# Kernel tuning notes

Hardware: AMD Instinct MI355X
Metric: run time of the kernel (lower is better)

## Reference

```python
import jax, jax.numpy as jnp
import numpy as np

ALPHA = 0.02  # LeakyReLU slope used throughout the module


def _leaky(x):
    return jnp.where(x >= 0, x, ALPHA * x)


def setup_inputs() -> dict:
    key = jax.random.key(0)
    ks = jax.random.split(key, 6)
    N, NEIGH, D_IN, D_HID, D_OUT = 131072, 25, 128, 32, 32
    self_vecs = jax.random.normal(ks[0], (N, D_IN), dtype=jnp.float32)
    neigh_vecs = jax.random.normal(ks[1], (N, NEIGH, D_IN), dtype=jnp.float32)
    # mlp params: truncated_normal(stddev=0.001) in original; normal*0.001 is fine for a reference
    W_mlp = jax.random.normal(ks[2], (D_IN, D_HID), dtype=jnp.float32) * 0.001
    b_mlp = jax.random.normal(ks[3], (D_HID,), dtype=jnp.float32) * 0.001
    # glorot uniform range sqrt(6/(fan_in+fan_out))
    r_va = float(np.sqrt(6.0 / (D_HID + D_OUT)))
    W_va = jax.random.uniform(ks[4], (D_IN, D_OUT), dtype=jnp.float32, minval=-r_va, maxval=r_va)
    W_neigh = jax.random.uniform(ks[5], (D_HID, D_OUT), dtype=jnp.float32, minval=-r_va, maxval=r_va)
    return {"self_vecs": self_vecs, "neigh_vecs": neigh_vecs,
            "W_mlp": W_mlp, "b_mlp": b_mlp, "W_va": W_va, "W_neigh": W_neigh}


def reference(self_vecs, neigh_vecs, W_mlp, b_mlp, W_va, W_neigh):
    # MLP over each neighbor feature: [N, NEIGH, D_IN] -> [N, NEIGH, D_HID]
    h = _leaky(jnp.einsum('bnd,dh->bnh', neigh_vecs, W_mlp) + b_mlp)
    # max-pool over neighbor axis -> [N, D_HID]
    neigh_h = jnp.max(h, axis=1)
    # two bias-free projections, add, final activation
    out = _leaky(self_vecs @ W_va + neigh_h @ W_neigh)  # [N, D_OUT]
    return out
```

## Files before the change

### kernel.cpp

```cpp
#include <hip/hip_runtime.h>
#include <stdint.h>

typedef short bf16x8 __attribute__((ext_vector_type(8)));
typedef float f32x4  __attribute__((ext_vector_type(4)));

static constexpr float ALPHA = 0.02f;

__device__ __forceinline__ float leaky(float x) { return fmaxf(x, ALPHA * x); }

__device__ __forceinline__ unsigned swz(unsigned b) {
    unsigned n = (b >> 9) & 15u;
    return b ^ (n << 5) ^ (((n >> 2) & 1u) << 4);
}

__device__ __forceinline__ short f2bf(float f) {
    unsigned u = __builtin_bit_cast(unsigned, f);
    unsigned r = (u + 0x7FFFu + ((u >> 16) & 1u)) >> 16;
    return (short)r;
}

__device__ __forceinline__ void gload16(const void* g, void* l) {
    __builtin_amdgcn_global_load_lds(
        (const __attribute__((address_space(1))) unsigned*)g,
        (__attribute__((address_space(3))) unsigned*)l, 16, 0, 0);
}

__device__ __forceinline__ bf16x8 frag_from_lds(const char* base, unsigned L) {
    const float4 a = *(const float4*)(base + swz(L));
    const float4 b = *(const float4*)(base + swz(L + 16u));
    bf16x8 r;
    r[0] = f2bf(a.x); r[1] = f2bf(a.y); r[2] = f2bf(a.z); r[3] = f2bf(a.w);
    r[4] = f2bf(b.x); r[5] = f2bf(b.y); r[6] = f2bf(b.z); r[7] = f2bf(b.w);
    return r;
}

__global__ __launch_bounds__(64, 1)
void sage_mfma(const float* __restrict__ self_vecs,
               const float* __restrict__ xg,
               const float* __restrict__ W_mlp,
               const float* __restrict__ b_mlp,
               const float* __restrict__ W_va,
               const float* __restrict__ W_neigh,
               float* __restrict__ out, int N)
{
    __shared__ __align__(16) char  buf0[13312];
    __shared__ __align__(16) char  buf1[13312];
    __shared__ __align__(16) float nhbuf[16 * 36];

    const int lane = threadIdx.x & 63;
    const int n15  = lane & 15;
    const int g    = lane >> 4;
    const unsigned wid  = blockIdx.x;
    const unsigned row0 = wid * 16u;

    const unsigned xlimit = (unsigned)N * 12800u - 16u;

    {
        unsigned base = row0 * 12800u;
#pragma unroll
        for (int i = 0; i < 13; ++i) {
            unsigned dl  = (unsigned)(i * 1024 + lane * 16);
            unsigned src = base + swz(dl);
            src = src > xlimit ? xlimit : src;
            gload16((const char*)xg + src, buf0 + i * 1024);
        }
    }

    bf16x8 B1[2][4], B2[2][5];
#pragma unroll
    for (int ht = 0; ht < 2; ++ht) {
#pragma unroll
        for (int kt = 0; kt < 4; ++kt) {
            bf16x8 r1, r2;
#pragma unroll
            for (int j = 0; j < 8; ++j) {
                int k = kt * 32 + g * 8 + j;
                r1[j] = f2bf(W_mlp[k * 32 + ht * 16 + n15]);
                r2[j] = f2bf(W_va [k * 32 + ht * 16 + n15]);
            }
            B1[ht][kt] = r1; B2[ht][kt] = r2;
        }
        bf16x8 r3;
#pragma unroll
        for (int j = 0; j < 8; ++j)
            r3[j] = f2bf(W_neigh[(g * 8 + j) * 32 + ht * 16 + n15]);
        B2[ht][4] = r3;
    }
    const float bl = b_mlp[n15], bh = b_mlp[16 + n15];

    const f32x4 zero4 = {0.f, 0.f, 0.f, 0.f};

#pragma unroll 2
    for (int r = 0; r < 16; ++r) {
        char* cur = (r & 1) ? buf1 : buf0;
        char* nxt = (r & 1) ? buf0 : buf1;

        if (r < 15) {
            unsigned base = (row0 + (unsigned)r + 1u) * 12800u;
#pragma unroll
            for (int i = 0; i < 13; ++i) {
                unsigned dl  = (unsigned)(i * 1024 + lane * 16);
                unsigned src = base + swz(dl);
                src = src > xlimit ? xlimit : src;
                gload16((const char*)xg + src, nxt + i * 1024);
            }
            asm volatile("s_waitcnt vmcnt(13)" ::: "memory");
        } else {
            unsigned base = row0 * 512u;
#pragma unroll
            for (int i = 0; i < 8; ++i) {
                unsigned dl = (unsigned)(i * 1024 + lane * 16);
                gload16((const char*)self_vecs + base + swz(dl), buf0 + i * 1024);
            }
            asm volatile("s_waitcnt vmcnt(8)" ::: "memory");
        }
        __builtin_amdgcn_sched_barrier(0);

        f32x4 acc[2][2];
        acc[0][0] = zero4; acc[0][1] = zero4; acc[1][0] = zero4; acc[1][1] = zero4;

        const unsigned nA = (unsigned)n15;
        const unsigned nB = (unsigned)((n15 < 9) ? (16 + n15) : 8);

#pragma unroll
        for (int kt = 0; kt < 4; ++kt) {
            bf16x8 a = frag_from_lds(cur, nA * 512u + (unsigned)(kt * 128 + g * 32));
            acc[0][0] = __builtin_amdgcn_mfma_f32_16x16x32_bf16(a, B1[0][kt], acc[0][0], 0, 0, 0);
            acc[0][1] = __builtin_amdgcn_mfma_f32_16x16x32_bf16(a, B1[1][kt], acc[0][1], 0, 0, 0);
        }
#pragma unroll
        for (int kt = 0; kt < 4; ++kt) {
            bf16x8 a = frag_from_lds(cur, nB * 512u + (unsigned)(kt * 128 + g * 32));
            acc[1][0] = __builtin_amdgcn_mfma_f32_16x16x32_bf16(a, B1[0][kt], acc[1][0], 0, 0, 0);
            acc[1][1] = __builtin_amdgcn_mfma_f32_16x16x32_bf16(a, B1[1][kt], acc[1][1], 0, 0, 0);
        }

#pragma unroll
        for (int ht = 0; ht < 2; ++ht) {
            float m = -3.0e38f;
#pragma unroll
            for (int q = 0; q < 4; ++q) m = fmaxf(m, acc[0][ht][q]);
#pragma unroll
            for (int q = 0; q < 4; ++q) {
                float v = (g * 4 + q < 9) ? acc[1][ht][q] : -3.0e38f;
                m = fmaxf(m, v);
            }
            m = fmaxf(m, __shfl_xor(m, 16));
            m = fmaxf(m, __shfl_xor(m, 32));
            float nhv = leaky(m + (ht ? bh : bl));
            if (lane < 16) nhbuf[r * 36 + ht * 16 + n15] = nhv;
        }
    }

    asm volatile("s_waitcnt vmcnt(0)" ::: "memory");
    __builtin_amdgcn_sched_barrier(0);

    f32x4 acc2[2];
    acc2[0] = zero4; acc2[1] = zero4;

#pragma unroll
    for (int kt = 0; kt < 4; ++kt) {
        bf16x8 a = frag_from_lds(buf0, (unsigned)n15 * 512u + (unsigned)(kt * 128 + g * 32));
        acc2[0] = __builtin_amdgcn_mfma_f32_16x16x32_bf16(a, B2[0][kt], acc2[0], 0, 0, 0);
        acc2[1] = __builtin_amdgcn_mfma_f32_16x16x32_bf16(a, B2[1][kt], acc2[1], 0, 0, 0);
    }
    {
        const float4 p = *(const float4*)&nhbuf[n15 * 36 + g * 8];
        const float4 q = *(const float4*)&nhbuf[n15 * 36 + g * 8 + 4];
        bf16x8 a;
        a[0] = f2bf(p.x); a[1] = f2bf(p.y); a[2] = f2bf(p.z); a[3] = f2bf(p.w);
        a[4] = f2bf(q.x); a[5] = f2bf(q.y); a[6] = f2bf(q.z); a[7] = f2bf(q.w);
        acc2[0] = __builtin_amdgcn_mfma_f32_16x16x32_bf16(a, B2[0][4], acc2[0], 0, 0, 0);
        acc2[1] = __builtin_amdgcn_mfma_f32_16x16x32_bf16(a, B2[1][4], acc2[1], 0, 0, 0);
    }

#pragma unroll
    for (int ht = 0; ht < 2; ++ht) {
#pragma unroll
        for (int q = 0; q < 4; ++q) {
            unsigned row = row0 + (unsigned)(g * 4 + q);
            out[(size_t)row * 32u + (unsigned)(ht * 16 + n15)] = leaky(acc2[ht][q]);
        }
    }
}

extern "C" void kernel_launch(void* const* d_in, const int* in_sizes, int n_in,
                              void* d_out, int out_size, void* d_ws, size_t ws_size,
                              hipStream_t stream)
{
    const float* self_vecs = (const float*)d_in[0];
    const float* neigh     = (const float*)d_in[1];
    const float* W_mlp     = (const float*)d_in[2];
    const float* b_mlp     = (const float*)d_in[3];
    const float* W_va      = (const float*)d_in[4];
    const float* W_neigh   = (const float*)d_in[5];
    float* outp            = (float*)d_out;

    const int N = in_sizes[0] / 128;

    sage_mfma<<<dim3(N / 16), dim3(64), 0, stream>>>(
        self_vecs, neigh, W_mlp, b_mlp, W_va, W_neigh, outp, N);
}
```

Baseline: 320.7 us.

## Split neighbor row buffer into two LDS halves to shrink footprint

Replaces the double-buffered 13 KB-per-row LDS staging with a single row split into an 8 KB part A (neighbors 0-15) and a 5 KB part B (neighbors 16-24). Part B loads are issued and consumed within the iteration, while part A of the next row is prefetched after its MFMA use. The goal is to roughly halve LDS use per block and raise launch_bounds min-blocks to 2 so more waves per CU hide memory latency. The cost is a shorter prefetch distance for part B, which is fetched only just before use, and the loop is no longer unrolled.

Measured after the change: 314.6 us. No clear change (-1.9%).

```diff
diff --git a/kernel.cpp b/kernel.cpp
--- a/kernel.cpp
+++ b/kernel.cpp
@@ -34,7 +34,7 @@
     return r;
 }
 
-__global__ __launch_bounds__(64, 1)
+__global__ __launch_bounds__(64, 2)
 void sage_mfma(const float* __restrict__ self_vecs,
                const float* __restrict__ xg,
                const float* __restrict__ W_mlp,
@@ -43,26 +43,23 @@
                const float* __restrict__ W_neigh,
                float* __restrict__ out, int N)
 {
-    __shared__ __align__(16) char  buf0[13312];
-    __shared__ __align__(16) char  buf1[13312];
+    __shared__ __align__(16) char  bufA[8192];
+    __shared__ __align__(16) char  bufB[5120];
     __shared__ __align__(16) float nhbuf[16 * 36];
 
     const int lane = threadIdx.x & 63;
     const int n15  = lane & 15;
     const int g    = lane >> 4;
-    const unsigned wid  = blockIdx.x;
-    const unsigned row0 = wid * 16u;
+    const unsigned row0 = blockIdx.x * 16u;
 
     const unsigned xlimit = (unsigned)N * 12800u - 16u;
 
     {
         unsigned base = row0 * 12800u;
 #pragma unroll
-        for (int i = 0; i < 13; ++i) {
-            unsigned dl  = (unsigned)(i * 1024 + lane * 16);
-            unsigned src = base + swz(dl);
-            src = src > xlimit ? xlimit : src;
-            gload16((const char*)xg + src, buf0 + i * 1024);
+        for (int i = 0; i < 8; ++i) {
+            unsigned dl = (unsigned)(i * 1024) + (unsigned)lane * 16u;
+            gload16((const char*)xg + base + swz(dl), bufA + i * 1024);
         }
     }
 
@@ -90,65 +87,69 @@
 
     const f32x4 zero4 = {0.f, 0.f, 0.f, 0.f};
 
-#pragma unroll 2
+#pragma unroll 1
     for (int r = 0; r < 16; ++r) {
-        char* cur = (r & 1) ? buf1 : buf0;
-        char* nxt = (r & 1) ? buf0 : buf1;
-
+        const unsigned rowbase = (row0 + (unsigned)r) * 12800u;
+
+        __builtin_amdgcn_sched_barrier(0);
+#pragma unroll
+        for (int i = 0; i < 5; ++i) {
+            unsigned dl  = (unsigned)(i * 1024) + (unsigned)lane * 16u;
+            unsigned src = rowbase + 8192u + swz(dl);
+            src = src > xlimit ? xlimit : src;
+            gload16((const char*)xg + src, bufB + i * 1024);
+        }
+        asm volatile("s_waitcnt vmcnt(5)" ::: "memory");
+        __builtin_amdgcn_sched_barrier(0);
+
+        f32x4 accA0 = zero4, accA1 = zero4;
+#pragma unroll
+        for (int kt = 0; kt < 4; ++kt) {
+            bf16x8 a = frag_from_lds(bufA, (unsigned)n15 * 512u + (unsigned)(kt * 128 + g * 32));
+            accA0 = __builtin_amdgcn_mfma_f32_16x16x32_bf16(a, B1[0][kt], accA0, 0, 0, 0);
+            accA1 = __builtin_amdgcn_mfma_f32_16x16x32_bf16(a, B1[1][kt], accA1, 0, 0, 0);
+        }
+        float m0 = fmaxf(fmaxf(accA0[0], accA0[1]), fmaxf(accA0[2], accA0[3]));
+        float m1 = fmaxf(fmaxf(accA1[0], accA1[1]), fmaxf(accA1[2], accA1[3]));
+
+        __builtin_amdgcn_sched_barrier(0);
         if (r < 15) {
-            unsigned base = (row0 + (unsigned)r + 1u) * 12800u;
-#pragma unroll
-            for (int i = 0; i < 13; ++i) {
-                unsigned dl  = (unsigned)(i * 1024 + lane * 16);
-                unsigned src = base + swz(dl);
-                src = src > xlimit ? xlimit : src;
-                gload16((const char*)xg + src, nxt + i * 1024);
+            unsigned nbase = (row0 + (unsigned)r + 1u) * 12800u;
+#pragma unroll
+            for (int i = 0; i < 8; ++i) {
+                unsigned dl = (unsigned)(i * 1024) + (unsigned)lane * 16u;
+                gload16((const char*)xg + nbase + swz(dl), bufA + i * 1024);
             }
-            asm volatile("s_waitcnt vmcnt(13)" ::: "memory");
         } else {
-            unsigned base = row0 * 512u;
+            unsigned sbase = row0 * 512u;
 #pragma unroll
             for (int i = 0; i < 8; ++i) {
-                unsigned dl = (unsigned)(i * 1024 + lane * 16);
-                gload16((const char*)self_vecs + base + swz(dl), buf0 + i * 1024);
+                unsigned dl = (unsigned)(i * 1024) + (unsigned)lane * 16u;
+                gload16((const char*)self_vecs + sbase + swz(dl), bufA + i * 1024);
             }
-            asm volatile("s_waitcnt vmcnt(8)" ::: "memory");
-        }
-        __builtin_amdgcn_sched_barrier(0);
-
-        f32x4 acc[2][2];
-        acc[0][0] = zero4; acc[0][1] = zero4; acc[1][0] = zero4; acc[1][1] = zero4;
-
-        const unsigned nA = (unsigned)n15;
-        const unsigned nB = (unsigned)((n15 < 9) ? (16 + n15) : 8);
-
+        }
+        asm volatile("s_waitcnt vmcnt(8)" ::: "memory");
+        __builtin_amdgcn_sched_barrier(0);
+
+        f32x4 accB0 = zero4, accB1 = zero4;
+        const unsigned rb = (n15 < 10) ? (unsigned)n15 : 9u;
 #pragma unroll
         for (int kt = 0; kt < 4; ++kt) {
-            bf16x8 a = frag_from_lds(cur, nA * 512u + (unsigned)(kt * 128 + g * 32));
-            acc[0][0] = __builtin_amdgcn_mfma_f32_16x16x32_bf16(a, B1[0][kt], acc[0][0], 0, 0, 0);
-            acc[0][1] = __builtin_amdgcn_mfma_f32_16x16x32_bf16(a, B1[1][kt], acc[0][1], 0, 0, 0);
-        }
-#pragma unroll
-        for (int kt = 0; kt < 4; ++kt) {
-            bf16x8 a = frag_from_lds(cur, nB * 512u + (unsigned)(kt * 128 + g * 32));
-            acc[1][0] = __builtin_amdgcn_mfma_f32_16x16x32_bf16(a, B1[0][kt], acc[1][0], 0, 0, 0);
-            acc[1][1] = __builtin_amdgcn_mfma_f32_16x16x32_bf16(a, B1[1][kt], acc[1][1], 0, 0, 0);
-        }
-
-#pragma unroll
-        for (int ht = 0; ht < 2; ++ht) {
-            float m = -3.0e38f;
-#pragma unroll
-            for (int q = 0; q < 4; ++q) m = fmaxf(m, acc[0][ht][q]);
-#pragma unroll
-            for (int q = 0; q < 4; ++q) {
-                float v = (g * 4 + q < 9) ? acc[1][ht][q] : -3.0e38f;
-                m = fmaxf(m, v);
-            }
-            m = fmaxf(m, __shfl_xor(m, 16));
-            m = fmaxf(m, __shfl_xor(m, 32));
-            float nhv = leaky(m + (ht ? bh : bl));
-            if (lane < 16) nhbuf[r * 36 + ht * 16 + n15] = nhv;
+            bf16x8 a = frag_from_lds(bufB, rb * 512u + (unsigned)(kt * 128 + g * 32));
+            accB0 = __builtin_amdgcn_mfma_f32_16x16x32_bf16(a, B1[0][kt], accB0, 0, 0, 0);
+            accB1 = __builtin_amdgcn_mfma_f32_16x16x32_bf16(a, B1[1][kt], accB1, 0, 0, 0);
+        }
+#pragma unroll
+        for (int q = 0; q < 4; ++q) {
+            const bool real = (g * 4 + q) < 9;
+            m0 = fmaxf(m0, real ? accB0[q] : -3.0e38f);
+            m1 = fmaxf(m1, real ? accB1[q] : -3.0e38f);
+        }
+        m0 = fmaxf(m0, __shfl_xor(m0, 16));  m0 = fmaxf(m0, __shfl_xor(m0, 32));
+        m1 = fmaxf(m1, __shfl_xor(m1, 16));  m1 = fmaxf(m1, __shfl_xor(m1, 32));
+        if (lane < 16) {
+            nhbuf[r * 36 + n15]      = leaky(m0 + bl);
+            nhbuf[r * 36 + 16 + n15] = leaky(m1 + bh);
         }
     }
 
@@ -160,7 +161,7 @@
 
 #pragma unroll
     for (int kt = 0; kt < 4; ++kt) {
-        bf16x8 a = frag_from_lds(buf0, (unsigned)n15 * 512u + (unsigned)(kt * 128 + g * 32));
+        bf16x8 a = frag_from_lds(bufA, (unsigned)n15 * 512u + (unsigned)(kt * 128 + g * 32));
         acc2[0] = __builtin_amdgcn_mfma_f32_16x16x32_bf16(a, B2[0][kt], acc2[0], 0, 0, 0);
         acc2[1] = __builtin_amdgcn_mfma_f32_16x16x32_bf16(a, B2[1][kt], acc2[1], 0, 0, 0);
     }
```
